# Optimization experiments

Hardware: AMD Instinct MI355X
Metric: run time of the kernel (lower is better)

The kernel has to match this reference:

```python
import jax, jax.numpy as jnp
import numpy as np

N = 2048       # total nodes in batch
G = 8          # graphs in batch
P_NODES = 256  # nodes per graph
E_PER_G = 2048 # directed random edges per graph (pre-symmetrization)
HID = 512
D = 512


def _lin(k, fi, fo):
    return jax.random.normal(k, (fi, fo), dtype=jnp.float32) * 0.05


def setup_inputs() -> dict:
    key = jax.random.key(0)
    ks = jax.random.split(key, 22)
    x = jax.random.normal(ks[0], (N, D), dtype=jnp.float32)
    # random intra-graph edges, no self-loops; symmetrized
    src = jax.random.randint(ks[1], (G, E_PER_G), 0, P_NODES)
    off = jax.random.randint(ks[2], (G, E_PER_G), 1, P_NODES)
    dst = (src + off) % P_NODES
    base = (jnp.arange(G) * P_NODES)[:, None]
    s = (src + base).reshape(-1)
    d = (dst + base).reshape(-1)
    edge_index = jnp.stack([jnp.concatenate([s, d]), jnp.concatenate([d, s])]).astype(jnp.int32)
    batch = jnp.repeat(jnp.arange(G, dtype=jnp.int32), P_NODES)
    inp = {"x": x, "edge_index": edge_index, "batch": batch}
    dims = [(1, HID, HID), (HID, HID, HID), (HID, HID, 1)]
    ki = 3
    for li, (i_, h_, o_) in enumerate(dims, 1):
        inp[f"w{li}1"] = _lin(ks[ki], i_, h_);   inp[f"b{li}1"] = jnp.zeros((h_,), jnp.float32)
        inp[f"w{li}2"] = _lin(ks[ki + 1], h_, h_); inp[f"b{li}2"] = jnp.zeros((h_,), jnp.float32)
        inp[f"w{li}3"] = _lin(ks[ki + 2], h_, o_); inp[f"b{li}3"] = jnp.zeros((o_,), jnp.float32)
        ki += 3
    return inp


def _mlp(h, w1, b1, w2, b2, w3, b3):
    # MLP.forward (enhance=False): relu(fc1) -> relu(fc2) -> sigmoid(fc3)
    h = jax.nn.relu(h @ w1 + b1)
    h = jax.nn.relu(h @ w2 + b2)
    return jax.nn.sigmoid(h @ w3 + b3)


def reference(x, edge_index, batch,
              w11, b11, w12, b12, w13, b13,
              w21, b21, w22, b22, w23, b23,
              w31, b31, w32, b32, w33, b33):
    n = x.shape[0]
    eye = jnp.eye(n, dtype=jnp.float32)
    # dense adjacency (A = diag(diag(L)) - L with L = D - A), unweighted, no self-loops
    A = jnp.zeros((n, n), jnp.float32).at[edge_index[0], edge_index[1]].set(1.0)
    A = A * (1.0 - eye)
    deg = A.sum(axis=1)
    # compute_entropy: V = x*(Lx) - x*(Ax) + A@(x*x), with Lx = deg*x - Ax
    Ax = A @ x
    V = x * (deg[:, None] * x - Ax) - x * Ax + A @ (x * x)
    Vn = jnp.linalg.norm(V, axis=1)
    # per-graph softmax over batch segments
    m = jax.ops.segment_max(Vn, batch, num_segments=G)
    e = jnp.exp(Vn - m[batch])
    Pn = e / jax.ops.segment_sum(e, batch, num_segments=G)[batch]
    Pn = jnp.where(Pn == 0.0, 1.0, Pn)  # P[P==0] += 1
    ent = (-Pn * jnp.log(Pn))[:, None]  # [N,1]
    # three GINConv layers (eps=0): MLP(x + A@x)
    h = _mlp(ent + A @ ent, w11, b11, w12, b12, w13, b13)
    h = _mlp(h + A @ h, w21, b21, w22, b22, w23, b23)
    h = _mlp(h + A @ h, w31, b31, w32, b32, w33, b33)
    prob = jax.nn.sigmoid(h)[:, 0]  # extra sigmoid as in forward()
    entf = ent[:, 0]
    gamma = entf.sum()
    loss = gamma - entf @ prob + prob @ (A @ prob)
    # greedy conditional expectation (sequential, sorted by prob desc)
    order = jnp.argsort(-prob)

    def step(carry, node):
        sel, rej, dummy = carry
        nb = A[node]                              # neighbor indicator row
        has_nb = nb.sum() > 0.0
        elig = jnp.logical_not(rej[node] | sel[node])
        s = (dummy * (1.0 - nb)).at[node].set(1.0)
        l = gamma - entf @ s + s @ (A @ s)
        take = has_nb & elig & (l <= loss)
        sel = sel.at[node].set(sel[node] | (~has_nb) | take)
        rej = jnp.where(take, rej | (nb > 0.0), rej)
        dummy = jnp.where(take, s, dummy)
        return (sel, rej, dummy), None

    init = (jnp.zeros(n, dtype=bool), jnp.zeros(n, dtype=bool), prob)
    (sel, _, _), _ = jax.lax.scan(step, init, order)
    # graph reconstruction: clamp(A^2 + A^3, 0, 1) with diagonal removed,
    # returned at full size masked by the selected-node mask (fixed shapes for jit)
    A2 = A @ A
    A3 = A2 @ A
    selm = sel.astype(jnp.float32)
    adj_pooled = jnp.clip(A2 + A3, 0.0, 1.0) * (1.0 - eye) * (selm[:, None] * selm[None, :])
    x_pooled = x * selm[:, None]
    return (x_pooled, adj_pooled, sel, loss)
```

## Files before the change

kernel.cpp:

```cpp
#include <hip/hip_runtime.h>
#include <stdint.h>

#define NN 2048
#define DD 512
#define NWORDS 8

typedef unsigned int u32;
typedef unsigned char u8;

__device__ __forceinline__ float sigmoidf_(float x){ return 1.0f/(1.0f+expf(-x)); }

__global__ void k_zero_bm(u32* bm){ int t = blockIdx.x*256+threadIdx.x; if(t<NN*NWORDS) bm[t]=0u; }

__global__ void k_scatter(const int* __restrict__ ei, u32* __restrict__ bm){
  int t = blockIdx.x*256+threadIdx.x;
  if(t>=32768) return;
  int r = ei[t];
  int c = ei[32768+t];
  atomicOr(&bm[r*NWORDS + ((c>>5)&7)], 1u<<(c&31));
}

__global__ void k_bm2_deg(const u32* __restrict__ bm, u32* __restrict__ bm2, int* __restrict__ deg){
  int r = blockIdx.x*256+threadIdx.x;
  if(r>=NN) return;
  int base = r & ~255;
  u32 acc[NWORDS];
  #pragma unroll
  for(int w=0;w<NWORDS;++w) acc[w]=0u;
  int d=0;
  #pragma unroll
  for(int w=0;w<NWORDS;++w){
    u32 m = bm[r*NWORDS+w];
    d += __popc(m);
    int b0 = w<<5;
    while(m){ int j=__ffs((int)m)-1; m&=m-1;
      const u32* row = bm + (size_t)(base+b0+j)*NWORDS;
      #pragma unroll
      for(int w2=0;w2<NWORDS;++w2) acc[w2] |= row[w2];
    }
  }
  #pragma unroll
  for(int w=0;w<NWORDS;++w) bm2[r*NWORDS+w]=acc[w];
  deg[r]=d;
}

__global__ void k_vn(const float* __restrict__ x, const u32* __restrict__ bm,
                     const int* __restrict__ deg, float* __restrict__ Vn){
  int node = blockIdx.x*4 + (threadIdx.x>>6);
  int lane = threadIdx.x & 63;
  int base = node & ~255;
  float degf = (float)deg[node];
  float ax[8], axx[8];
  #pragma unroll
  for(int k=0;k<8;++k){ ax[k]=0.0f; axx[k]=0.0f; }
  #pragma unroll
  for(int w=0;w<NWORDS;++w){
    u32 m = bm[node*NWORDS+w]; int b0=w<<5;
    while(m){ int j=__ffs((int)m)-1; m&=m-1;
      const float* xr = x + (size_t)(base+b0+j)*DD;
      #pragma unroll
      for(int k=0;k<8;++k){ float v = xr[lane+64*k]; ax[k]+=v; axx[k]=fmaf(v,v,axx[k]); }
    }
  }
  const float* xi = x + (size_t)node*DD;
  double vn2 = 0.0;
  #pragma unroll
  for(int k=0;k<8;++k){
    float xf = xi[lane+64*k];
    float val = xf*(degf*xf - ax[k]) - xf*ax[k] + axx[k];
    vn2 += (double)val*(double)val;
  }
  #pragma unroll
  for(int off=32;off>0;off>>=1) vn2 += __shfl_down(vn2, off);
  if(lane==0) Vn[node] = (float)sqrt(vn2);
}

__global__ void k_softent(const float* __restrict__ Vn, float* __restrict__ ent){
  __shared__ float red[4];
  __shared__ float sh;
  int g = blockIdx.x, tid = threadIdx.x;
  float v = Vn[g*256+tid];
  float m = v;
  #pragma unroll
  for(int off=32;off>0;off>>=1) m = fmaxf(m, __shfl_down(m,off));
  if((tid&63)==0) red[tid>>6]=m;
  __syncthreads();
  if(tid==0) sh = fmaxf(fmaxf(red[0],red[1]),fmaxf(red[2],red[3]));
  __syncthreads();
  float mx = sh;
  float e = expf(v-mx);
  float s = e;
  #pragma unroll
  for(int off=32;off>0;off>>=1) s += __shfl_down(s,off);
  if((tid&63)==0) red[tid>>6]=s;
  __syncthreads();
  if(tid==0) sh = red[0]+red[1]+red[2]+red[3];
  __syncthreads();
  float Pn = e / sh;
  if(Pn==0.0f) Pn=1.0f;
  ent[g*256+tid] = -Pn*logf(Pn);
}

__global__ void k_u(const u32* __restrict__ bm, const float* __restrict__ ent, float* __restrict__ uo){
  int i = blockIdx.x*256+threadIdx.x;
  if(i>=NN) return;
  int base = i & ~255;
  float acc = ent[i];
  #pragma unroll
  for(int w=0;w<NWORDS;++w){
    u32 m = bm[i*NWORDS+w]; int b0=w<<5;
    while(m){ int j=__ffs((int)m)-1; m&=m-1; acc += ent[base+b0+j]; }
  }
  uo[i]=acc;
}

__global__ void k_h1(const float* __restrict__ u, const float* __restrict__ w11,
                     const float* __restrict__ b11, float* __restrict__ h){
  int t = blockIdx.x*256+threadIdx.x;
  if(t>=NN*DD) return;
  int i = t>>9; int f = t&511;
  h[t] = fmaxf(fmaf(u[i], w11[f], b11[f]), 0.0f);
}

template<int ACT>
__global__ __launch_bounds__(256) void k_gemm(const float* __restrict__ A, const float* __restrict__ B,
                                              const float* __restrict__ bias, float* __restrict__ C){
  __shared__ float As[32][68];
  __shared__ float Bs[32][68];
  int tid = threadIdx.x;
  int m0 = blockIdx.x*64;
  int n0 = blockIdx.y*64;
  int ty = tid>>4, tx = tid&15;
  float acc[4][4];
  #pragma unroll
  for(int i=0;i<4;++i){
    #pragma unroll
    for(int j=0;j<4;++j) acc[i][j]=0.0f;
  }
  for(int k0=0;k0<512;k0+=32){
    __syncthreads();
    #pragma unroll
    for(int t0=0;t0<2;++t0){
      int t = tid + t0*256;
      int row = t>>3, c4 = t&7;
      float4 v = *(const float4*)(A + (size_t)(m0+row)*512 + k0 + c4*4);
      As[c4*4+0][row]=v.x; As[c4*4+1][row]=v.y; As[c4*4+2][row]=v.z; As[c4*4+3][row]=v.w;
    }
    #pragma unroll
    for(int t0=0;t0<2;++t0){
      int t = tid + t0*256;
      int row = t>>4, c4 = t&15;
      float4 v = *(const float4*)(B + (size_t)(k0+row)*512 + n0 + c4*4);
      *(float4*)&Bs[row][c4*4] = v;
    }
    __syncthreads();
    #pragma unroll
    for(int kk=0;kk<32;++kk){
      float4 a = *(const float4*)&As[kk][ty*4];
      float4 b = *(const float4*)&Bs[kk][tx*4];
      float av[4]={a.x,a.y,a.z,a.w}, bv[4]={b.x,b.y,b.z,b.w};
      #pragma unroll
      for(int i=0;i<4;++i){
        #pragma unroll
        for(int j=0;j<4;++j) acc[i][j] = fmaf(av[i],bv[j],acc[i][j]);
      }
    }
  }
  #pragma unroll
  for(int i=0;i<4;++i){
    float4 o;
    float* oo = &o.x;
    #pragma unroll
    for(int j=0;j<4;++j){
      float v = acc[i][j] + bias[n0+tx*4+j];
      if(ACT==0) v = fmaxf(v,0.0f);
      else      v = 1.0f/(1.0f+expf(-v));
      oo[j]=v;
    }
    *(float4*)(C + (size_t)(m0+ty*4+i)*512 + n0 + tx*4) = o;
  }
}

__global__ void k_spmm_add(const float* __restrict__ h, const u32* __restrict__ bm, float* __restrict__ out){
  int node = blockIdx.x*4 + (threadIdx.x>>6);
  int lane = threadIdx.x & 63;
  int base = node & ~255;
  float acc[8];
  #pragma unroll
  for(int k=0;k<8;++k) acc[k] = h[(size_t)node*DD + lane + 64*k];
  #pragma unroll
  for(int w=0;w<NWORDS;++w){
    u32 m = bm[node*NWORDS+w]; int b0=w<<5;
    while(m){ int j=__ffs((int)m)-1; m&=m-1;
      const float* hr = h + (size_t)(base+b0+j)*DD;
      #pragma unroll
      for(int k=0;k<8;++k) acc[k] += hr[lane+64*k];
    }
  }
  #pragma unroll
  for(int k=0;k<8;++k) out[(size_t)node*DD + lane + 64*k] = acc[k];
}

__global__ void k_gemv_prob(const float* __restrict__ h, const float* __restrict__ w33,
                            const float* __restrict__ b33, float* __restrict__ prob){
  int node = blockIdx.x*4 + (threadIdx.x>>6);
  int lane = threadIdx.x & 63;
  float acc = 0.0f;
  #pragma unroll
  for(int k=0;k<8;++k) acc = fmaf(h[(size_t)node*512 + lane + 64*k], w33[lane+64*k], acc);
  #pragma unroll
  for(int off=32;off>0;off>>=1) acc += __shfl_down(acc, off);
  if(lane==0){
    float z = sigmoidf_(acc + b33[0]);
    prob[node] = sigmoidf_(z);
  }
}

__global__ void k_sort(const float* __restrict__ prob, int* __restrict__ order){
  __shared__ float kp[NN];
  __shared__ int ki[NN];
  int tid = threadIdx.x;
  for(int t=tid;t<NN;t+=1024){ kp[t]=prob[t]; ki[t]=t; }
  __syncthreads();
  for(int k=2;k<=NN;k<<=1){
    for(int j=k>>1;j>0;j>>=1){
      for(int t=tid;t<NN;t+=1024){
        int l = t ^ j;
        if(l > t){
          bool up = ((t & k) == 0);
          float pa=kp[t]; int ia=ki[t]; float pb=kp[l]; int ib=ki[l];
          bool before_ab = (pa > pb) || (pa == pb && ia < ib);
          bool dosw = up ? (!before_ab) : before_ab;
          if(dosw){ kp[t]=pb; ki[t]=ib; kp[l]=pa; ki[l]=ia; }
        }
      }
      __syncthreads();
    }
  }
  for(int t=tid;t<NN;t+=1024) order[t]=ki[t];
}

__device__ __forceinline__ double block_reduce_d(double v, double* red, int tid){
  #pragma unroll
  for(int off=32;off>0;off>>=1) v += __shfl_down(v, off);
  if((tid&63)==0) red[tid>>6]=v;
  __syncthreads();
  double r=0.0;
  if(tid==0) r = red[0]+red[1]+red[2]+red[3];
  return r;
}

__global__ void k_scan(const u32* __restrict__ bm, const int* __restrict__ deg,
                       const float* __restrict__ ent, const float* __restrict__ prob,
                       const int* __restrict__ order, float* __restrict__ selw,
                       float* __restrict__ out_sel, float* __restrict__ out_loss){
  extern __shared__ char smem[];
  double* dsc = (double*)smem;
  double* red = dsc + 12;
  u32* bm_s = (u32*)(red + 4);
  float* dummy_s = (float*)(bm_s + NN*NWORDS);
  float* entf_s = dummy_s + NN;
  float* sbuf = entf_s + NN;
  int* order_s = (int*)(sbuf + 256);
  int* ctl = order_s + NN;
  u8* sel_s = (u8*)(ctl + 4);
  u8* rej_s = sel_s + NN;
  int tid = threadIdx.x;

  for(int t=tid;t<NN*NWORDS;t+=256) bm_s[t]=bm[t];
  for(int t=tid;t<NN;t+=256){
    dummy_s[t]=prob[t];
    entf_s[t]=ent[t];
    order_s[t]=order[t];
    sel_s[t] = (deg[t]==0)?1:0;
    rej_s[t]=0;
  }
  __syncthreads();

  double gl=0.0;
  for(int t=tid;t<NN;t+=256) gl += (double)entf_s[t];
  gl = block_reduce_d(gl, red, tid);
  if(tid==0){ dsc[0]=gl; dsc[2]=0.0; }
  __syncthreads();

  for(int g=0;g<8;++g){
    int base=g<<8;
    float sc = dummy_s[base+tid];
    sbuf[tid]=sc;
    __syncthreads();
    double As=0.0;
    {
      const u32* row = bm_s + (size_t)(base+tid)*NWORDS;
      #pragma unroll
      for(int w=0;w<NWORDS;++w){ u32 m=row[w]; int b0=w<<5;
        while(m){ int j=__ffs((int)m)-1; m&=m-1; As += (double)sbuf[b0+j]; } }
    }
    double val = (double)sc*As - (double)entf_s[base+tid]*(double)sc;
    val = block_reduce_d(val, red, tid);
    if(tid==0){ dsc[3+g]=val; dsc[2]+=val; }
    __syncthreads();
  }
  if(tid==0){ dsc[1]=dsc[0]+dsc[2]; out_loss[0]=(float)dsc[1]; }
  __syncthreads();

  for(int t=0;t<NN;++t){
    if(tid==0){
      int node = order_s[t];
      ctl[0] = (!sel_s[node] && !rej_s[node]) ? 1 : 0;
      ctl[1] = node;
    }
    __syncthreads();
    if(ctl[0]){
      int node = ctl[1];
      int base = node & ~255;
      int r = node & 255;
      u32 w = bm_s[(size_t)node*NWORDS + (tid>>5)];
      int isnb = (w >> (tid&31)) & 1;
      float sc = (tid==r) ? 1.0f : (isnb ? 0.0f : dummy_s[base+tid]);
      sbuf[tid]=sc;
      __syncthreads();
      double As=0.0;
      {
        const u32* row = bm_s + (size_t)(base+tid)*NWORDS;
        #pragma unroll
        for(int ww=0;ww<NWORDS;++ww){ u32 m=row[ww]; int b0=ww<<5;
          while(m){ int j=__ffs((int)m)-1; m&=m-1; As += (double)sbuf[b0+j]; } }
      }
      double val = (double)sc*As - (double)entf_s[base+tid]*(double)sc;
      val = block_reduce_d(val, red, tid);
      if(tid==0){
        int g = node>>8;
        double l = dsc[0] + dsc[2] - dsc[3+g] + val;
        int take = (l <= dsc[1]) ? 1 : 0;
        if(take){ dsc[2] += val - dsc[3+g]; dsc[3+g]=val; sel_s[node]=1; }
        ctl[2]=take;
      }
      __syncthreads();
      if(ctl[2]){
        dummy_s[base+tid]=sbuf[tid];
        if(isnb) rej_s[base+tid]=1;
      }
      __syncthreads();
    }
  }

  for(int t=tid;t<NN;t+=256){
    float sv = sel_s[t]?1.0f:0.0f;
    selw[t]=sv; out_sel[t]=sv;
  }
}

__global__ void k_xpool(const float* __restrict__ x, const float* __restrict__ selw, float* __restrict__ out){
  int t = blockIdx.x*256+threadIdx.x;
  if(t >= NN*(DD/4)) return;
  int i = t >> 7;
  float s = selw[i];
  float4 v = ((const float4*)x)[t];
  v.x*=s; v.y*=s; v.z*=s; v.w*=s;
  ((float4*)out)[t] = v;
}

__global__ void k_adj(const u32* __restrict__ bm, const u32* __restrict__ bm2,
                      const float* __restrict__ selw, float* __restrict__ outadj){
  int r = blockIdx.x;
  int c = blockIdx.y*256 + threadIdx.x;
  float val = 0.0f;
  if ((r>>8)==(c>>8) && r!=c && selw[r]!=0.0f && selw[c]!=0.0f){
    int lc = c & 255;
    u32 any = (bm2[r*NWORDS + (lc>>5)] >> (lc&31)) & 1u;
    if(!any){
      #pragma unroll
      for(int w=0;w<NWORDS;++w) any |= (bm2[r*NWORDS+w] & bm[c*NWORDS+w]);
    }
    val = any ? 1.0f : 0.0f;
  }
  outadj[(size_t)r*2048 + c] = val;
}

extern "C" void kernel_launch(void* const* d_in, const int* in_sizes, int n_in,
                              void* d_out, int out_size, void* d_ws, size_t ws_size,
                              hipStream_t stream){
  const float* x  = (const float*)d_in[0];
  const int* ei   = (const int*)d_in[1];
  const float* w11=(const float*)d_in[3];  const float* b11=(const float*)d_in[4];
  const float* w12=(const float*)d_in[5];  const float* b12=(const float*)d_in[6];
  const float* w13=(const float*)d_in[7];  const float* b13=(const float*)d_in[8];
  const float* w21=(const float*)d_in[9];  const float* b21=(const float*)d_in[10];
  const float* w22=(const float*)d_in[11]; const float* b22=(const float*)d_in[12];
  const float* w23=(const float*)d_in[13]; const float* b23=(const float*)d_in[14];
  const float* w31=(const float*)d_in[15]; const float* b31=(const float*)d_in[16];
  const float* w32=(const float*)d_in[17]; const float* b32=(const float*)d_in[18];
  const float* w33=(const float*)d_in[19]; const float* b33=(const float*)d_in[20];

  char* ws = (char*)d_ws;
  u32* bm    = (u32*)(ws + 0);
  u32* bm2   = (u32*)(ws + 65536);
  int* deg   = (int*)(ws + 131072);
  float* Vn  = (float*)(ws + 139264);
  float* ent = (float*)(ws + 147456);
  float* uarr= (float*)(ws + 155648);
  float* prob= (float*)(ws + 163840);
  int* order = (int*)(ws + 172032);
  float* selw= (float*)(ws + 180224);
  float* buf0= (float*)(ws + (1<<20));
  float* buf1= (float*)(ws + (1<<20) + (size_t)NN*DD*4);

  float* out = (float*)d_out;
  float* out_xp   = out;
  float* out_adj  = out + 1048576;
  float* out_sel  = out + 1048576 + 4194304;
  float* out_loss = out + 1048576 + 4194304 + 2048;

  hipFuncSetAttribute((const void*)k_scan, hipFuncAttributeMaxDynamicSharedMemorySize, 98304);

  k_zero_bm<<<64,256,0,stream>>>(bm);
  k_scatter<<<128,256,0,stream>>>(ei, bm);
  k_bm2_deg<<<8,256,0,stream>>>(bm, bm2, deg);
  k_vn<<<512,256,0,stream>>>(x, bm, deg, Vn);
  k_softent<<<8,256,0,stream>>>(Vn, ent);
  k_u<<<8,256,0,stream>>>(bm, ent, uarr);
  k_h1<<<4096,256,0,stream>>>(uarr, w11, b11, buf0);
  dim3 gg(32,8);
  k_gemm<0><<<gg,256,0,stream>>>(buf0, w12, b12, buf1);
  k_gemm<1><<<gg,256,0,stream>>>(buf1, w13, b13, buf0);
  k_spmm_add<<<512,256,0,stream>>>(buf0, bm, buf1);
  k_gemm<0><<<gg,256,0,stream>>>(buf1, w21, b21, buf0);
  k_gemm<0><<<gg,256,0,stream>>>(buf0, w22, b22, buf1);
  k_gemm<1><<<gg,256,0,stream>>>(buf1, w23, b23, buf0);
  k_spmm_add<<<512,256,0,stream>>>(buf0, bm, buf1);
  k_gemm<0><<<gg,256,0,stream>>>(buf1, w31, b31, buf0);
  k_gemm<0><<<gg,256,0,stream>>>(buf0, w32, b32, buf1);
  k_gemv_prob<<<512,256,0,stream>>>(buf1, w33, b33, prob);
  k_sort<<<1,1024,0,stream>>>(prob, order);
  k_scan<<<1,256,95376,stream>>>(bm, deg, ent, prob, order, selw, out_sel, out_loss);
  k_xpool<<<1024,256,0,stream>>>(x, selw, out_xp);
  dim3 ga(2048,8);
  k_adj<<<ga,256,0,stream>>>(bm, bm2, selw, out_adj);
}
```

Baseline: 1.854 ms.

## Rewrite greedy scan as single-wavefront incremental loss updates with cached A·dummy

Moves the sequential greedy selection onto one 64-lane wavefront and computes each candidate's change in loss incrementally. It keeps y = A·dummy in shared memory, touches only the candidate's neighbourhood, and updates y locally when a node is taken. Rejected and selected state is held as register bitmasks exchanged through shuffles, so skipped nodes cost no block barriers. The old per-step full 256-row SpMV and the block-wide reductions with several __syncthreads per step are gone. The price is a new k_y precompute kernel, more shared memory, and possible floating-point differences from the reordered incremental summation.

```diff
diff --git a/kernel.cpp b/kernel.cpp
--- a/kernel.cpp
+++ b/kernel.cpp
@@ -214,6 +214,32 @@
     float z = sigmoidf_(acc + b33[0]);
     prob[node] = sigmoidf_(z);
   }
+}
+
+__global__ __launch_bounds__(256) void k_y(const u32* __restrict__ bm, const float* __restrict__ prob,
+                 const float* __restrict__ ent, double* __restrict__ y,
+                 double* __restrict__ cg, double* __restrict__ gam){
+  __shared__ float p_s[256];
+  __shared__ double redc[4], redg[4];
+  int g = blockIdx.x, i = threadIdx.x;
+  int node = (g<<8) + i;
+  float p = prob[node];
+  p_s[i] = p;
+  __syncthreads();
+  double acc = 0.0;
+  #pragma unroll
+  for (int w = 0; w < NWORDS; ++w){
+    u32 m = bm[(size_t)node*NWORDS + w];
+    while (m){ int j=__ffs((int)m)-1; m&=m-1; acc += (double)p_s[(w<<5)+j]; }
+  }
+  y[node] = acc;
+  double e = (double)ent[node];
+  double c = (double)p*acc - e*(double)p;
+  #pragma unroll
+  for (int off=32; off>0; off>>=1){ c += __shfl_down(c,off); e += __shfl_down(e,off); }
+  if ((i&63)==0){ redc[i>>6]=c; redg[i>>6]=e; }
+  __syncthreads();
+  if (i==0){ cg[g]=redc[0]+redc[1]+redc[2]+redc[3]; gam[g]=redg[0]+redg[1]+redg[2]+redg[3]; }
 }
 
 __global__ void k_sort(const float* __restrict__ prob, int* __restrict__ order){
@@ -240,113 +266,127 @@
   for(int t=tid;t<NN;t+=1024) order[t]=ki[t];
 }
 
-__device__ __forceinline__ double block_reduce_d(double v, double* red, int tid){
-  #pragma unroll
-  for(int off=32;off>0;off>>=1) v += __shfl_down(v, off);
-  if((tid&63)==0) red[tid>>6]=v;
-  __syncthreads();
-  double r=0.0;
-  if(tid==0) r = red[0]+red[1]+red[2]+red[3];
-  return r;
-}
-
-__global__ void k_scan(const u32* __restrict__ bm, const int* __restrict__ deg,
-                       const float* __restrict__ ent, const float* __restrict__ prob,
-                       const int* __restrict__ order, float* __restrict__ selw,
-                       float* __restrict__ out_sel, float* __restrict__ out_loss){
+__global__ void __launch_bounds__(64) k_scan(const u32* __restrict__ bm, const int* __restrict__ deg,
+    const float* __restrict__ ent, const float* __restrict__ prob, const int* __restrict__ order,
+    const double* __restrict__ yg, const double* __restrict__ cgp, const double* __restrict__ gamp,
+    float* __restrict__ selw, float* __restrict__ out_sel, float* __restrict__ out_loss)
+{
   extern __shared__ char smem[];
-  double* dsc = (double*)smem;
-  double* red = dsc + 12;
-  u32* bm_s = (u32*)(red + 4);
+  u32* bm_s      = (u32*)smem;
   float* dummy_s = (float*)(bm_s + NN*NWORDS);
-  float* entf_s = dummy_s + NN;
-  float* sbuf = entf_s + NN;
-  int* order_s = (int*)(sbuf + 256);
-  int* ctl = order_s + NN;
-  u8* sel_s = (u8*)(ctl + 4);
-  u8* rej_s = sel_s + NN;
-  int tid = threadIdx.x;
-
-  for(int t=tid;t<NN*NWORDS;t+=256) bm_s[t]=bm[t];
-  for(int t=tid;t<NN;t+=256){
-    dummy_s[t]=prob[t];
-    entf_s[t]=ent[t];
-    order_s[t]=order[t];
-    sel_s[t] = (deg[t]==0)?1:0;
-    rej_s[t]=0;
-  }
-  __syncthreads();
-
-  double gl=0.0;
-  for(int t=tid;t<NN;t+=256) gl += (double)entf_s[t];
-  gl = block_reduce_d(gl, red, tid);
-  if(tid==0){ dsc[0]=gl; dsc[2]=0.0; }
-  __syncthreads();
-
-  for(int g=0;g<8;++g){
-    int base=g<<8;
-    float sc = dummy_s[base+tid];
-    sbuf[tid]=sc;
-    __syncthreads();
-    double As=0.0;
-    {
-      const u32* row = bm_s + (size_t)(base+tid)*NWORDS;
-      #pragma unroll
-      for(int w=0;w<NWORDS;++w){ u32 m=row[w]; int b0=w<<5;
-        while(m){ int j=__ffs((int)m)-1; m&=m-1; As += (double)sbuf[b0+j]; } }
-    }
-    double val = (double)sc*As - (double)entf_s[base+tid]*(double)sc;
-    val = block_reduce_d(val, red, tid);
-    if(tid==0){ dsc[3+g]=val; dsc[2]+=val; }
-    __syncthreads();
-  }
-  if(tid==0){ dsc[1]=dsc[0]+dsc[2]; out_loss[0]=(float)dsc[1]; }
-  __syncthreads();
-
-  for(int t=0;t<NN;++t){
-    if(tid==0){
-      int node = order_s[t];
-      ctl[0] = (!sel_s[node] && !rej_s[node]) ? 1 : 0;
-      ctl[1] = node;
-    }
-    __syncthreads();
-    if(ctl[0]){
-      int node = ctl[1];
-      int base = node & ~255;
-      int r = node & 255;
-      u32 w = bm_s[(size_t)node*NWORDS + (tid>>5)];
-      int isnb = (w >> (tid&31)) & 1;
-      float sc = (tid==r) ? 1.0f : (isnb ? 0.0f : dummy_s[base+tid]);
-      sbuf[tid]=sc;
+  float* entf_s  = dummy_s + NN;
+  double* y_s    = (double*)(entf_s + NN);
+  int* order_s   = (int*)(y_s + NN);
+  float* u_scr   = (float*)(order_s + NN);
+  int lane = threadIdx.x;
+
+  for (int t = lane; t < NN*NWORDS; t += 64) bm_s[t] = bm[t];
+  for (int t = lane; t < NN; t += 64){
+    dummy_s[t] = prob[t];
+    entf_s[t]  = ent[t];
+    y_s[t]     = yg[t];
+    order_s[t] = order[t];
+  }
+  u32 myDead = 0, mySel = 0;
+  #pragma unroll 4
+  for (int k = 0; k < 32; ++k){
+    int node = lane*32 + k;
+    if (deg[node] == 0){ myDead |= 1u<<k; mySel |= 1u<<k; }
+  }
+  double totC = 0.0, gamma = 0.0;
+  #pragma unroll
+  for (int g = 0; g < 8; ++g){ totC += cgp[g]; gamma += gamp[g]; }
+  const double loss = gamma + totC;
+  if (lane == 0) out_loss[0] = (float)loss;
+  __syncthreads();
+
+  int nxt = order_s[0];
+  for (int t = 0; t < NN; ++t){
+    int node = nxt;
+    if (t+1 < NN) nxt = order_s[t+1];
+    u32 dw = __shfl(myDead, node>>5);
+    if ((dw >> (node&31)) & 1u) continue;
+
+    int g = node >> 8, base = node & ~255, r = node & 255;
+    u32 rv[8];
+    #pragma unroll
+    for (int w = 0; w < 8; ++w) rv[w] = bm_s[node*NWORDS + w];
+    float dv = dummy_s[node];
+    float uv = 1.0f - dv;
+
+    double dsum = 0.0, accU = 0.0;
+    float uc_[4];
+    #pragma unroll
+    for (int q = 0; q < 4; ++q){
+      int c = lane*4 + q;
+      int isnb = (rv[c>>5] >> (c&31)) & 1;
+      float d = dummy_s[base + c];
+      float uc = 0.0f;
+      if (c == r) uc = uv;
+      else if (isnb) uc = -d;
+      uc_[q] = uc;
+      if (uc != 0.0f)
+        dsum += (double)uc * (2.0*y_s[base+c] - (double)entf_s[base+c]);
+      if (isnb){
+        accU -= (double)d;
+        double ps = 0.0;
+        #pragma unroll
+        for (int w = 0; w < 8; ++w){
+          u32 m = bm_s[(size_t)(base+c)*NWORDS + w] & rv[w];
+          while (m){ int j=__ffs((int)m)-1; m&=m-1; ps += (double)dummy_s[base + (w<<5) + j]; }
+        }
+        dsum += (double)d * ps;
+      }
+    }
+    #pragma unroll
+    for (int off = 1; off < 64; off <<= 1){
+      dsum += __shfl_xor(dsum, off);
+      accU += __shfl_xor(accU, off);
+    }
+    double delta = dsum + 2.0 * (double)uv * accU;
+
+    if (gamma + totC + delta <= loss){
+      totC += delta;
+      #pragma unroll
+      for (int q = 0; q < 4; ++q){
+        int c = lane*4 + q;
+        u_scr[c] = uc_[q];
+        if (uc_[q] != 0.0f) dummy_s[base+c] = (c==r) ? 1.0f : 0.0f;
+      }
+      if (lane == (node>>5)) mySel |= 1u << (node&31);
+      {
+        int w = lane - g*8;
+        if (w >= 0 && w < 8){
+          u32 sm = rv[w];
+          if (w == (r>>5)) sm |= 1u << (r&31);
+          myDead |= sm;
+        }
+      }
       __syncthreads();
-      double As=0.0;
-      {
-        const u32* row = bm_s + (size_t)(base+tid)*NWORDS;
+      u32 suppm[8];
+      #pragma unroll
+      for (int w = 0; w < 8; ++w) suppm[w] = rv[w];
+      suppm[r>>5] |= 1u << (r&31);
+      #pragma unroll
+      for (int q = 0; q < 4; ++q){
+        int c = lane*4 + q;
+        double dy = 0.0;
         #pragma unroll
-        for(int ww=0;ww<NWORDS;++ww){ u32 m=row[ww]; int b0=ww<<5;
-          while(m){ int j=__ffs((int)m)-1; m&=m-1; As += (double)sbuf[b0+j]; } }
-      }
-      double val = (double)sc*As - (double)entf_s[base+tid]*(double)sc;
-      val = block_reduce_d(val, red, tid);
-      if(tid==0){
-        int g = node>>8;
-        double l = dsc[0] + dsc[2] - dsc[3+g] + val;
-        int take = (l <= dsc[1]) ? 1 : 0;
-        if(take){ dsc[2] += val - dsc[3+g]; dsc[3+g]=val; sel_s[node]=1; }
-        ctl[2]=take;
+        for (int w = 0; w < 8; ++w){
+          u32 m = bm_s[(size_t)(base+c)*NWORDS + w] & suppm[w];
+          while (m){ int j=__ffs((int)m)-1; m&=m-1; dy += (double)u_scr[(w<<5)+j]; }
+        }
+        if (dy != 0.0) y_s[base+c] += dy;
       }
       __syncthreads();
-      if(ctl[2]){
-        dummy_s[base+tid]=sbuf[tid];
-        if(isnb) rej_s[base+tid]=1;
-      }
-      __syncthreads();
-    }
-  }
-
-  for(int t=tid;t<NN;t+=256){
-    float sv = sel_s[t]?1.0f:0.0f;
-    selw[t]=sv; out_sel[t]=sv;
+    }
+  }
+
+  #pragma unroll 4
+  for (int k = 0; k < 32; ++k){
+    int node = lane*32 + k;
+    float sv = ((mySel >> k) & 1u) ? 1.0f : 0.0f;
+    selw[node] = sv; out_sel[node] = sv;
   }
 }
 
@@ -402,6 +442,9 @@
   float* prob= (float*)(ws + 163840);
   int* order = (int*)(ws + 172032);
   float* selw= (float*)(ws + 180224);
+  double* yg = (double*)(ws + 196608);
+  double* cg = (double*)(ws + 212992);
+  double* gam= (double*)(ws + 213056);
   float* buf0= (float*)(ws + (1<<20));
   float* buf1= (float*)(ws + (1<<20) + (size_t)NN*DD*4);
 
@@ -411,7 +454,7 @@
   float* out_sel  = out + 1048576 + 4194304;
   float* out_loss = out + 1048576 + 4194304 + 2048;
 
-  hipFuncSetAttribute((const void*)k_scan, hipFuncAttributeMaxDynamicSharedMemorySize, 98304);
+  hipFuncSetAttribute((const void*)k_scan, hipFuncAttributeMaxDynamicSharedMemorySize, 107520);
 
   k_zero_bm<<<64,256,0,stream>>>(bm);
   k_scatter<<<128,256,0,stream>>>(ei, bm);
@@ -431,8 +474,9 @@
   k_gemm<0><<<gg,256,0,stream>>>(buf1, w31, b31, buf0);
   k_gemm<0><<<gg,256,0,stream>>>(buf0, w32, b32, buf1);
   k_gemv_prob<<<512,256,0,stream>>>(buf1, w33, b33, prob);
+  k_y<<<8,256,0,stream>>>(bm, prob, ent, yg, cg, gam);
   k_sort<<<1,1024,0,stream>>>(prob, order);
-  k_scan<<<1,256,95376,stream>>>(bm, deg, ent, prob, order, selw, out_sel, out_loss);
+  k_scan<<<1,64,107520,stream>>>(bm, deg, ent, prob, order, yg, cg, gam, selw, out_sel, out_loss);
   k_xpool<<<1024,256,0,stream>>>(x, selw, out_xp);
   dim3 ga(2048,8);
   k_adj<<<ga,256,0,stream>>>(bm, bm2, selw, out_adj);
```

Result: slower. 2.862 ms (+54.4%).
